# Kernel tuning notes

Measured on AMD Instinct MI355X. Metric: run time of the kernel, lower is better.

Reference implementation:

```python
import jax, jax.numpy as jnp
import numpy as np

D_MODEL, H, G = 2048, 32, 8
D_K = D_MODEL // H          # 64
GROUP_SIZE = H // G         # 4
B, S = 2, 2048


def setup_inputs() -> dict:
    key = jax.random.key(0)
    ks = jax.random.split(key, 9)
    sd = 1.0 / np.sqrt(D_MODEL)
    x = jax.random.normal(ks[0], (B, S, D_MODEL), dtype=jnp.float32)
    Wq = jax.random.normal(ks[1], (D_MODEL, D_MODEL), dtype=jnp.float32) * sd
    bq = jax.random.normal(ks[2], (D_MODEL,), dtype=jnp.float32) * 0.01
    Wk = jax.random.normal(ks[3], (D_MODEL, G * D_K), dtype=jnp.float32) * sd
    bk = jax.random.normal(ks[4], (G * D_K,), dtype=jnp.float32) * 0.01
    Wv = jax.random.normal(ks[5], (D_MODEL, G * D_K), dtype=jnp.float32) * sd
    bv = jax.random.normal(ks[6], (G * D_K,), dtype=jnp.float32) * 0.01
    Wo = jax.random.normal(ks[7], (D_MODEL, D_MODEL), dtype=jnp.float32) * sd
    bo = jax.random.normal(ks[8], (D_MODEL,), dtype=jnp.float32) * 0.01
    return {"x": x, "Wq": Wq, "bq": bq, "Wk": Wk, "bk": bk,
            "Wv": Wv, "bv": bv, "Wo": Wo, "bo": bo}


def reference(x, Wq, bq, Wk, bk, Wv, bv, Wo, bo):
    Bsz, Sln, _ = x.shape
    # projections
    Q = (x @ Wq + bq).reshape(Bsz, Sln, H, D_K).transpose(0, 2, 1, 3)   # [B,h,S,dk]
    K = (x @ Wk + bk).reshape(Bsz, Sln, G, D_K).transpose(0, 2, 1, 3)   # [B,g,S,dk]
    V = (x @ Wv + bv).reshape(Bsz, Sln, G, D_K).transpose(0, 2, 1, 3)   # [B,g,S,dk]
    # reshape Q into groups: [B, g, group_size, S, dk]; K/V broadcast over group dim
    Qg = Q.reshape(Bsz, G, GROUP_SIZE, Sln, D_K)
    scores = jnp.einsum('bgmqd,bgkd->bgmqk', Qg, K) / jnp.sqrt(jnp.float32(D_K))
    attn = jax.nn.softmax(scores, axis=-1)                              # [B,g,gs,S,S]
    out = jnp.einsum('bgmqk,bgkd->bgmqd', attn, V)                      # [B,g,gs,S,dk]
    out = out.reshape(Bsz, H, Sln, D_K).transpose(0, 2, 1, 3).reshape(Bsz, Sln, D_MODEL)
    return out @ Wo + bo
```

## Files before the change

kernel.cpp:

```cpp
#include <hip/hip_runtime.h>
#include <stdint.h>

#define DMODEL 2048
#define NHEADS 32
#define NGRP 8
#define DKH 64
#define BATCH 2
#define SEQ 2048
#define MTOT (BATCH*SEQ)

typedef unsigned short u16;
typedef __bf16 bf16x8 __attribute__((ext_vector_type(8)));
typedef float f32x4 __attribute__((ext_vector_type(4)));
typedef _Float16 f16x4 __attribute__((ext_vector_type(4)));
typedef _Float16 f16x2 __attribute__((ext_vector_type(2)));

#define QSCALE 0.18033688011112042f

__device__ __forceinline__ u16 f2bf(float f){
    uint32_t x = __float_as_uint(f);
    x += 0x7FFFu + ((x >> 16) & 1u);
    return (u16)(x >> 16);
}

__device__ __forceinline__ void gld_lds16(const u16* g, u16* l){
    __builtin_amdgcn_global_load_lds(
        (const __attribute__((address_space(1))) uint32_t*)g,
        (__attribute__((address_space(3))) uint32_t*)l, 16, 0, 0);
}


__global__ void cvt_x_kern(const float* __restrict__ x, u16* __restrict__ xb){
    int i = (blockIdx.x * 256 + threadIdx.x) * 4;
    float4 v = *(const float4*)(x + i);
    uint32_t lo = (uint32_t)f2bf(v.x) | ((uint32_t)f2bf(v.y) << 16);
    uint32_t hi = (uint32_t)f2bf(v.z) | ((uint32_t)f2bf(v.w) << 16);
    *(uint2*)(xb + i) = make_uint2(lo, hi);
}

__global__ void cvt_wT_all(const float* __restrict__ Wq, const float* __restrict__ Wk,
                           const float* __restrict__ Wv, const float* __restrict__ Wo,
                           u16* __restrict__ WqT, u16* __restrict__ WkT,
                           u16* __restrict__ WvT, u16* __restrict__ WoT){
    __shared__ float t[32][33];
    int bx = blockIdx.x;
    const float* W; u16* T; int N; int cx;
    if (bx < 64)      { W = Wq; T = WqT; N = 2048; cx = bx; }
    else if (bx < 80) { W = Wk; T = WkT; N = 512;  cx = bx - 64; }
    else if (bx < 96) { W = Wv; T = WvT; N = 512;  cx = bx - 80; }
    else              { W = Wo; T = WoT; N = 2048; cx = bx - 96; }
    int tx = threadIdx.x & 31, ty = threadIdx.x >> 5;
    int n0 = cx * 32, k0 = blockIdx.y * 32;
#pragma unroll
    for (int i = 0; i < 4; i++)
        t[ty*4+i][tx] = W[(size_t)(k0 + ty*4 + i) * N + n0 + tx];
    __syncthreads();
#pragma unroll
    for (int i = 0; i < 4; i++)
        T[(size_t)(n0 + ty*4 + i) * DMODEL + k0 + tx] = f2bf(t[tx][ty*4+i]);
}

template<int EPI>
__global__ __launch_bounds__(256, 2) void gemm_nt(
    const u16* __restrict__ A, const u16* __restrict__ Bt,
    const float* __restrict__ bias0, const float* __restrict__ bias1, const float* __restrict__ bias2,
    void* __restrict__ out0, void* __restrict__ out1, void* __restrict__ out2, int Kn)
{
    __shared__ alignas(16) u16 As[128*32];
    __shared__ alignas(16) u16 Bs[128*32];
    const int tid  = threadIdx.x;
    const int w    = tid >> 6, lane = tid & 63, quad = lane >> 4, l16 = lane & 15;
    const int wr   = w >> 1,  wc   = w & 1;
    const int m0   = blockIdx.x * 128, n0 = blockIdx.y * 128;
    const int arow = lane >> 2, acol = (lane & 3) * 8;

    const u16* ga = A  + (size_t)(m0 + w*32 + arow) * Kn + acol;
    const u16* gb = Bt + (size_t)(n0 + w*32 + arow) * Kn + acol;
    u16* la = As + (w*32) * 32;
    u16* lb = Bs + (w*32) * 32;

    f32x4 acc[4][4] = {};

    for (int k0 = 0; k0 < Kn; k0 += 32){
        __syncthreads();
        gld_lds16(ga + k0,                  la);
        gld_lds16(ga + k0 + (size_t)16*Kn,  la + 16*32);
        gld_lds16(gb + k0,                  lb);
        gld_lds16(gb + k0 + (size_t)16*Kn,  lb + 16*32);
        __syncthreads();
        bf16x8 af[4], bfr[4];
#pragma unroll
        for (int t = 0; t < 4; t++)
            af[t]  = *(const bf16x8*)(As + (wr*64 + t*16 + l16)*32 + quad*8);
#pragma unroll
        for (int t = 0; t < 4; t++)
            bfr[t] = *(const bf16x8*)(Bs + (wc*64 + t*16 + l16)*32 + quad*8);
#pragma unroll
        for (int tm = 0; tm < 4; tm++)
#pragma unroll
            for (int tn = 0; tn < 4; tn++)
                acc[tm][tn] = __builtin_amdgcn_mfma_f32_16x16x32_bf16(af[tm], bfr[tn], acc[tm][tn], 0, 0, 0);
    }

#pragma unroll
    for (int tn = 0; tn < 4; tn++){
        int col = n0 + wc*64 + tn*16 + l16;
        float bv;
        if (EPI == 3) bv = (col < 2048) ? bias0[col] : (col < 2560) ? bias1[col-2048] : bias2[col-2560];
        else          bv = bias0[col];
#pragma unroll
        for (int tm = 0; tm < 4; tm++){
#pragma unroll
            for (int r = 0; r < 4; r++){
                int row = m0 + wr*64 + tm*16 + quad*4 + r;
                float v = acc[tm][tn][r] + bv;
                if (EPI == 3){
                    int b = row >> 11, s = row & (SEQ-1);
                    if (col < 2048){
                        int hh = col >> 6, d = col & 63;
                        ((u16*)out0)[(((size_t)b*NHEADS + hh)*SEQ + s)*DKH + d] = f2bf(v * QSCALE);
                    } else if (col < 2560){
                        int c = col - 2048, gg = c >> 6, d = c & 63;
                        ((u16*)out1)[(((size_t)b*NGRP + gg)*SEQ + s)*DKH + d] = f2bf(v);
                    } else {
                        int c = col - 2560, gg = c >> 6, d = c & 63;
                        ((u16*)out2)[(((size_t)b*NGRP + gg)*DKH + d)*SEQ + s] =
                            __builtin_bit_cast(u16, (_Float16)v);
                    }
                } else {
                    ((float*)out0)[(size_t)row * DMODEL + col] = v;
                }
            }
        }
    }
}

__global__ __launch_bounds__(512, 2) void flash_kern(
    const u16* __restrict__ Qb, const u16* __restrict__ Kb,
    const u16* __restrict__ Vt, u16* __restrict__ Ob)
{
    __shared__ alignas(16) u16 Ks[2][64*64];
    __shared__ alignas(16) u16 Vs[2][64*64];
    const int tid = threadIdx.x, w = tid >> 6, lane = tid & 63;
    const int quad = lane >> 4, l16 = lane & 15;
    const int q0 = blockIdx.x * 512;
    const int h  = blockIdx.y, b = blockIdx.z, g = h >> 2;

    const u16* Qg = Qb + (((size_t)b*NHEADS + h)*SEQ + q0 + w*64) * DKH;
    const u16* Kg = Kb + ((size_t)b*NGRP + g) * SEQ * DKH;
    const u16* Vg = Vt + ((size_t)b*NGRP + g) * DKH * SEQ;

    const int lr = lane >> 3, lc = lane & 7;
    const int sw = lc ^ lr;
    const u16* gk0 = Kg + (size_t)(w*8 + lr) * DKH + sw*8;
    const u16* gv0 = Vg + (size_t)(w*8 + lr) * SEQ + sw*8;

    bf16x8 aq[2][4];
#pragma unroll
    for (int nt = 0; nt < 4; nt++)
#pragma unroll
        for (int ks = 0; ks < 2; ks++)
            aq[ks][nt] = *(const bf16x8*)(Qg + (nt*16 + l16)*DKH + ks*32 + quad*8);

    float lsum[4] = {};
    f32x4 oa[4][4] = {};

#define STAGE(buf, kt) do{                                            \
        gld_lds16(gk0 + (size_t)(kt)*64*DKH, Ks[buf] + (w*8)*64);     \
        gld_lds16(gv0 + (size_t)(kt)*64,     Vs[buf] + (w*8)*64);     \
    }while(0)

#define COMPUTE(buf) do{                                                              \
        _Pragma("unroll")                                                             \
        for (int kc = 0; kc < 4; kc++){                                               \
            bf16x8 bk0 = *(const bf16x8*)(Ks[buf] + (kc*16 + l16)*64                  \
                                          + ((quad     ^ (l16&7)) * 8));              \
            bf16x8 bk1 = *(const bf16x8*)(Ks[buf] + (kc*16 + l16)*64                  \
                                          + (((4+quad) ^ (l16&7)) * 8));              \
            f16x4 pa[4];                                                              \
            _Pragma("unroll")                                                         \
            for (int nt = 0; nt < 4; nt++){                                           \
                f32x4 sa = {};                                                        \
                sa = __builtin_amdgcn_mfma_f32_16x16x32_bf16(bk0, aq[0][nt], sa,0,0,0);\
                sa = __builtin_amdgcn_mfma_f32_16x16x32_bf16(bk1, aq[1][nt], sa,0,0,0);\
                float e0 = __builtin_amdgcn_exp2f(sa[0]);                             \
                float e1 = __builtin_amdgcn_exp2f(sa[1]);                             \
                float e2 = __builtin_amdgcn_exp2f(sa[2]);                             \
                float e3 = __builtin_amdgcn_exp2f(sa[3]);                             \
                lsum[nt] += (e0 + e1) + (e2 + e3);                                    \
                uint2 pk = make_uint2(                                                \
                    __builtin_bit_cast(uint32_t, __builtin_amdgcn_cvt_pkrtz(e0, e1)), \
                    __builtin_bit_cast(uint32_t, __builtin_amdgcn_cvt_pkrtz(e2, e3)));\
                pa[nt] = __builtin_bit_cast(f16x4, pk);                               \
            }                                                                         \
            _Pragma("unroll")                                                         \
            for (int dt = 0; dt < 4; dt++){                                           \
                f16x4 bv = *(const f16x4*)(Vs[buf] + (dt*16 + l16)*64                 \
                             + (((2*kc + (quad>>1)) ^ (l16&7)) * 8) + (quad&1)*4);    \
                _Pragma("unroll")                                                     \
                for (int nt = 0; nt < 4; nt++)                                        \
                    oa[nt][dt] = __builtin_amdgcn_mfma_f32_16x16x16f16(               \
                        pa[nt], bv, oa[nt][dt], 0, 0, 0);                             \
            }                                                                         \
        }                                                                             \
    }while(0)

    STAGE(0, 0);
    __syncthreads();

    for (int kt2 = 0; kt2 < SEQ/128; ++kt2){
        int kt = kt2 * 2;
        STAGE(1, kt + 1);
        COMPUTE(0);
        __syncthreads();
        if (kt2 < SEQ/128 - 1) STAGE(0, kt + 2);
        COMPUTE(1);
        __syncthreads();
    }

#pragma unroll
    for (int nt = 0; nt < 4; nt++){
        float s = lsum[nt];
        s += __shfl_xor(s, 16, 64);
        s += __shfl_xor(s, 32, 64);
        lsum[nt] = 1.0f / s;
    }

#pragma unroll
    for (int nt = 0; nt < 4; nt++)
#pragma unroll
        for (int r = 0; r < 4; r++){
            float inv = __shfl(lsum[nt], quad*4 + r, 64);
            int q = q0 + w*64 + nt*16 + quad*4 + r;
#pragma unroll
            for (int dt = 0; dt < 4; dt++)
                Ob[((size_t)b*SEQ + q)*DMODEL + h*DKH + dt*16 + l16] = f2bf(oa[nt][dt][r] * inv);
        }
#undef STAGE
#undef COMPUTE
}


extern "C" void kernel_launch(void* const* d_in, const int* in_sizes, int n_in,
                              void* d_out, int out_size, void* d_ws, size_t ws_size,
                              hipStream_t stream)
{
    const float* x  = (const float*)d_in[0];
    const float* Wq = (const float*)d_in[1];
    const float* bq = (const float*)d_in[2];
    const float* Wk = (const float*)d_in[3];
    const float* bk = (const float*)d_in[4];
    const float* Wv = (const float*)d_in[5];
    const float* bv = (const float*)d_in[6];
    const float* Wo = (const float*)d_in[7];
    const float* bo = (const float*)d_in[8];

    uint8_t* p = (uint8_t*)d_ws;
    u16* xb  = (u16*)p; p += (size_t)MTOT*DMODEL*2;
    u16* WqT = (u16*)p; p += (size_t)DMODEL*DMODEL*2;
    u16* WkT = (u16*)p; p += (size_t)(NGRP*DKH)*DMODEL*2;
    u16* WvT = (u16*)p; p += (size_t)(NGRP*DKH)*DMODEL*2;
    u16* WoT = (u16*)p; p += (size_t)DMODEL*DMODEL*2;
    u16* Qb  = (u16*)p; p += (size_t)BATCH*NHEADS*SEQ*DKH*2;
    u16* Kb  = (u16*)p; p += (size_t)BATCH*NGRP*SEQ*DKH*2;
    u16* Vtb = (u16*)p; p += (size_t)BATCH*NGRP*DKH*SEQ*2;
    u16* Ob  = (u16*)p; p += (size_t)MTOT*DMODEL*2;

    cvt_x_kern<<<MTOT*DMODEL/1024, 256, 0, stream>>>(x, xb);
    cvt_wT_all<<<dim3(160, 64), 256, 0, stream>>>(Wq, Wk, Wv, Wo, WqT, WkT, WvT, WoT);

    gemm_nt<3><<<dim3(MTOT/128, 3072/128), 256, 0, stream>>>(
        xb, WqT, bq, bk, bv, Qb, Kb, Vtb, DMODEL);

    flash_kern<<<dim3(SEQ/512, NHEADS, BATCH), 512, 0, stream>>>(Qb, Kb, Vtb, Ob);

    gemm_nt<2><<<dim3(MTOT/128, DMODEL/128), 256, 0, stream>>>(
        Ob, WoT, bo, nullptr, nullptr, d_out, nullptr, nullptr, DMODEL);
}
```

Before: 319.6 us.

## Use 16x16x32 f16 MFMA for PV and halve flash query tile per wave

The PV product now uses the K=32 f16 MFMA. Two half-chunks of P fragments are packed into f16x8 operands, with a permuted key-row mapping for the QK step so the score layout lines up with V columns. Each wave now handles 32 queries instead of 64, which doubles the grid and raises launch bounds to 4 blocks per SM for occupancy. The aim is fewer MFMA issues and better latency hiding, at the cost of more K/V reloads per query and more blocks sharing LDS.

```diff
diff --git a/kernel.cpp b/kernel.cpp
--- a/kernel.cpp
+++ b/kernel.cpp
@@ -12,8 +12,7 @@
 typedef unsigned short u16;
 typedef __bf16 bf16x8 __attribute__((ext_vector_type(8)));
 typedef float f32x4 __attribute__((ext_vector_type(4)));
-typedef _Float16 f16x4 __attribute__((ext_vector_type(4)));
-typedef _Float16 f16x2 __attribute__((ext_vector_type(2)));
+typedef _Float16 f16x8 __attribute__((ext_vector_type(8)));
 
 #define QSCALE 0.18033688011112042f
 
@@ -135,7 +134,7 @@
     }
 }
 
-__global__ __launch_bounds__(512, 2) void flash_kern(
+__global__ __launch_bounds__(512, 4) void flash_kern(
     const u16* __restrict__ Qb, const u16* __restrict__ Kb,
     const u16* __restrict__ Vt, u16* __restrict__ Ob)
 {
@@ -143,10 +142,10 @@
     __shared__ alignas(16) u16 Vs[2][64*64];
     const int tid = threadIdx.x, w = tid >> 6, lane = tid & 63;
     const int quad = lane >> 4, l16 = lane & 15;
-    const int q0 = blockIdx.x * 512;
+    const int q0 = blockIdx.x * 256;
     const int h  = blockIdx.y, b = blockIdx.z, g = h >> 2;
 
-    const u16* Qg = Qb + (((size_t)b*NHEADS + h)*SEQ + q0 + w*64) * DKH;
+    const u16* Qg = Qb + (((size_t)b*NHEADS + h)*SEQ + q0 + w*32) * DKH;
     const u16* Kg = Kb + ((size_t)b*NGRP + g) * SEQ * DKH;
     const u16* Vg = Vt + ((size_t)b*NGRP + g) * DKH * SEQ;
 
@@ -155,15 +154,18 @@
     const u16* gk0 = Kg + (size_t)(w*8 + lr) * DKH + sw*8;
     const u16* gv0 = Vg + (size_t)(w*8 + lr) * SEQ + sw*8;
 
-    bf16x8 aq[2][4];
-#pragma unroll
-    for (int nt = 0; nt < 4; nt++)
+    bf16x8 aq[2][2];
+#pragma unroll
+    for (int nt = 0; nt < 2; nt++)
 #pragma unroll
         for (int ks = 0; ks < 2; ks++)
             aq[ks][nt] = *(const bf16x8*)(Qg + (nt*16 + l16)*DKH + ks*32 + quad*8);
 
-    float lsum[4] = {};
-    f32x4 oa[4][4] = {};
+    const int krbase = ((l16 >> 2) * 8) + (l16 & 3);
+    const int rx     = l16 & 3;
+
+    float lsum[2] = {};
+    f32x4 oa[2][4] = {};
 
 #define STAGE(buf, kt) do{                                            \
         gld_lds16(gk0 + (size_t)(kt)*64*DKH, Ks[buf] + (w*8)*64);     \
@@ -172,34 +174,42 @@
 
 #define COMPUTE(buf) do{                                                              \
         _Pragma("unroll")                                                             \
-        for (int kc = 0; kc < 4; kc++){                                               \
-            bf16x8 bk0 = *(const bf16x8*)(Ks[buf] + (kc*16 + l16)*64                  \
-                                          + ((quad     ^ (l16&7)) * 8));              \
-            bf16x8 bk1 = *(const bf16x8*)(Ks[buf] + (kc*16 + l16)*64                  \
-                                          + (((4+quad) ^ (l16&7)) * 8));              \
-            f16x4 pa[4];                                                              \
+        for (int c2 = 0; c2 < 2; c2++){                                               \
+            uint2 ph[2][2];                            \
             _Pragma("unroll")                                                         \
-            for (int nt = 0; nt < 4; nt++){                                           \
-                f32x4 sa = {};                                                        \
-                sa = __builtin_amdgcn_mfma_f32_16x16x32_bf16(bk0, aq[0][nt], sa,0,0,0);\
-                sa = __builtin_amdgcn_mfma_f32_16x16x32_bf16(bk1, aq[1][nt], sa,0,0,0);\
-                float e0 = __builtin_amdgcn_exp2f(sa[0]);                             \
-                float e1 = __builtin_amdgcn_exp2f(sa[1]);                             \
-                float e2 = __builtin_amdgcn_exp2f(sa[2]);                             \
-                float e3 = __builtin_amdgcn_exp2f(sa[3]);                             \
-                lsum[nt] += (e0 + e1) + (e2 + e3);                                    \
-                uint2 pk = make_uint2(                                                \
-                    __builtin_bit_cast(uint32_t, __builtin_amdgcn_cvt_pkrtz(e0, e1)), \
-                    __builtin_bit_cast(uint32_t, __builtin_amdgcn_cvt_pkrtz(e2, e3)));\
-                pa[nt] = __builtin_bit_cast(f16x4, pk);                               \
+            for (int hf = 0; hf < 2; hf++){                                           \
+                const u16* krow = Ks[buf] + (c2*32 + krbase + hf*4)*64;               \
+                int cx = rx + hf*4;                                                   \
+                bf16x8 bk0 = *(const bf16x8*)(krow + ((quad     ^ cx) * 8));          \
+                bf16x8 bk1 = *(const bf16x8*)(krow + (((4+quad) ^ cx) * 8));          \
+                _Pragma("unroll")                                                     \
+                for (int nt = 0; nt < 2; nt++){                                       \
+                    f32x4 sa = {};                                                    \
+                    sa = __builtin_amdgcn_mfma_f32_16x16x32_bf16(bk0, aq[0][nt], sa,0,0,0); \
+                    sa = __builtin_amdgcn_mfma_f32_16x16x32_bf16(bk1, aq[1][nt], sa,0,0,0); \
+                    float e0 = __builtin_amdgcn_exp2f(sa[0]);                         \
+                    float e1 = __builtin_amdgcn_exp2f(sa[1]);                         \
+                    float e2 = __builtin_amdgcn_exp2f(sa[2]);                         \
+                    float e3 = __builtin_amdgcn_exp2f(sa[3]);                         \
+                    lsum[nt] += (e0 + e1) + (e2 + e3);                                \
+                    ph[hf][nt] = make_uint2(                                          \
+                        __builtin_bit_cast(uint32_t, __builtin_amdgcn_cvt_pkrtz(e0, e1)), \
+                        __builtin_bit_cast(uint32_t, __builtin_amdgcn_cvt_pkrtz(e2, e3)));\
+                }                                                                     \
+            }                                                                         \
+            f16x8 pa[2];                                                              \
+            _Pragma("unroll")                                                         \
+            for (int nt = 0; nt < 2; nt++){                                           \
+                uint4 u = make_uint4(ph[0][nt].x, ph[0][nt].y, ph[1][nt].x, ph[1][nt].y); \
+                pa[nt] = __builtin_bit_cast(f16x8, u);                                \
             }                                                                         \
             _Pragma("unroll")                                                         \
             for (int dt = 0; dt < 4; dt++){                                           \
-                f16x4 bv = *(const f16x4*)(Vs[buf] + (dt*16 + l16)*64                 \
-                             + (((2*kc + (quad>>1)) ^ (l16&7)) * 8) + (quad&1)*4);    \
+                f16x8 bv = *(const f16x8*)(Vs[buf] + (dt*16 + l16)*64                 \
+                                           + (((c2*4 + quad) ^ (l16&7)) * 8));        \
                 _Pragma("unroll")                                                     \
-                for (int nt = 0; nt < 4; nt++)                                        \
-                    oa[nt][dt] = __builtin_amdgcn_mfma_f32_16x16x16f16(               \
+                for (int nt = 0; nt < 2; nt++)                                        \
+                    oa[nt][dt] = __builtin_amdgcn_mfma_f32_16x16x32_f16(              \
                         pa[nt], bv, oa[nt][dt], 0, 0, 0);                             \
             }                                                                         \
         }                                                                             \
@@ -219,7 +229,7 @@
     }
 
 #pragma unroll
-    for (int nt = 0; nt < 4; nt++){
+    for (int nt = 0; nt < 2; nt++){
         float s = lsum[nt];
         s += __shfl_xor(s, 16, 64);
         s += __shfl_xor(s, 32, 64);
@@ -227,11 +237,11 @@
     }
 
 #pragma unroll
-    for (int nt = 0; nt < 4; nt++)
+    for (int nt = 0; nt < 2; nt++)
 #pragma unroll
         for (int r = 0; r < 4; r++){
             float inv = __shfl(lsum[nt], quad*4 + r, 64);
-            int q = q0 + w*64 + nt*16 + quad*4 + r;
+            int q = q0 + w*32 + nt*16 + quad*4 + r;
 #pragma unroll
             for (int dt = 0; dt < 4; dt++)
                 Ob[((size_t)b*SEQ + q)*DMODEL + h*DKH + dt*16 + l16] = f2bf(oa[nt][dt][r] * inv);
@@ -272,7 +282,7 @@
     gemm_nt<3><<<dim3(MTOT/128, 3072/128), 256, 0, stream>>>(
         xb, WqT, bq, bk, bv, Qb, Kb, Vtb, DMODEL);
 
-    flash_kern<<<dim3(SEQ/512, NHEADS, BATCH), 512, 0, stream>>>(Qb, Kb, Vtb, Ob);
+    flash_kern<<<dim3(SEQ/256, NHEADS, BATCH), 512, 0, stream>>>(Qb, Kb, Vtb, Ob);
 
     gemm_nt<2><<<dim3(MTOT/128, DMODEL/128), 256, 0, stream>>>(
         Ob, WoT, bo, nullptr, nullptr, d_out, nullptr, nullptr, DMODEL);
```

New measurement: 332.8 us. +4.1%, slower.
